# Kernel tuning notes

Hardware: AMD Instinct MI355X
Metric: run time of the kernel (lower is better)

Reference implementation:

```python
import jax, jax.numpy as jnp
import numpy as np

B, T, F = 8, 4096, 256

def setup_inputs() -> dict:
    key = jax.random.key(0)
    ks = jax.random.split(key, 10)
    s = 1.0 / np.sqrt(F)
    return {
        "x": jax.random.normal(ks[0], (B, T, F), dtype=jnp.float32),
        "Wq_w": jax.random.normal(ks[1], (F, F), dtype=jnp.float32) * s,
        "Wq_b": jax.random.normal(ks[2], (F,), dtype=jnp.float32) * 0.01,
        "Wk_w": jax.random.normal(ks[3], (F, F), dtype=jnp.float32) * s,
        "Wk_b": jax.random.normal(ks[4], (F,), dtype=jnp.float32) * 0.01,
        "Wv_w": jax.random.normal(ks[5], (F, F), dtype=jnp.float32) * s,
        "Wv_b": jax.random.normal(ks[6], (F,), dtype=jnp.float32) * 0.01,
        "w": jax.random.normal(ks[7], (T, T), dtype=jnp.float32) * 0.02,
        "out_w": jax.random.normal(ks[8], (F, F), dtype=jnp.float32) * s,
        "out_b": jax.random.normal(ks[9], (F,), dtype=jnp.float32) * 0.01,
    }

def reference(x, Wq_w, Wq_b, Wk_w, Wk_b, Wv_w, Wv_b, w, out_w, out_b):
    # Linear layers (torch convention: y = x @ W.T + b)
    Q = x @ Wq_w.T + Wq_b                      # [B, T, F]
    K = x @ Wk_w.T + Wk_b                      # [B, T, F]
    V = x @ Wv_w.T + Wv_b                      # [B, T, F]
    Q_sig = jax.nn.sigmoid(Q)
    # Stabilized exponentials (faithful: w over rows, K over FEATURE dim)
    exp_w = jnp.exp(w - jnp.max(w, axis=-1, keepdims=True))        # [T, T]
    exp_K = jnp.exp(K - jnp.max(K, axis=-1, keepdims=True))        # [B, T, F]
    num = jnp.einsum('ts,bsf->btf', exp_w, exp_K * V)              # [B, T, F]
    den = jnp.einsum('ts,bsf->btf', exp_w, exp_K)                  # [B, T, F]
    Yt = Q_sig * (num / den)
    return Yt @ out_w.T + out_b
```

## Files before the change

### kernel.cpp

```cpp
#include <hip/hip_runtime.h>
#include <hip/hip_bf16.h>

#define BB 8
#define TT 4096
#define FF 256
#define BT 32768

typedef unsigned short u16;
typedef __attribute__((ext_vector_type(8))) short short8;
typedef __attribute__((ext_vector_type(4))) float f32x4;
typedef __attribute__((ext_vector_type(4))) unsigned int u32x4;

static __device__ __forceinline__ float bf2f(u16 u) {
    union { unsigned int i; float f; } v; v.i = ((unsigned int)u) << 16; return v.f;
}
static __device__ __forceinline__ u16 f2bf(float f) {
    union { float f; unsigned int i; } v; v.f = f;
    unsigned int x = v.i;
    return (u16)((x + 0x7fffu + ((x >> 16) & 1u)) >> 16);
}

typedef const __attribute__((address_space(1))) void gvoid_t;
typedef __attribute__((address_space(3))) void svoid_t;

__global__ __launch_bounds__(256) void expw_kernel(const float* __restrict__ w,
                                                   u16* __restrict__ ew) {
    __shared__ float red[256];
    int row = blockIdx.x;
    int tid = threadIdx.x;
    const float* wr = w + (size_t)row * TT;

    f32x4 vals[4];
    float m = -1e30f;
#pragma unroll
    for (int v = 0; v < 4; ++v) {
        int idx = (v * 256 + tid) * 4;
        vals[v] = *(const f32x4*)(wr + idx);
#pragma unroll
        for (int j = 0; j < 4; ++j) m = fmaxf(m, vals[v][j]);
    }
    red[tid] = m;
    __syncthreads();
    for (int s = 128; s > 0; s >>= 1) {
        if (tid < s) red[tid] = fmaxf(red[tid], red[tid + s]);
        __syncthreads();
    }
    float rm = red[0];
#pragma unroll
    for (int v = 0; v < 4; ++v) {
        int idx = (v * 256 + tid) * 4;
        float e0 = expf(vals[v][0] - rm), e1 = expf(vals[v][1] - rm);
        float e2 = expf(vals[v][2] - rm), e3 = expf(vals[v][3] - rm);
        uint2 pk;
        pk.x = (unsigned int)f2bf(e0) | ((unsigned int)f2bf(e1) << 16);
        pk.y = (unsigned int)f2bf(e2) | ((unsigned int)f2bf(e3) << 16);
        *(uint2*)(ew + (size_t)row * TT + idx) = pk;
    }
}

__global__ __launch_bounds__(256) void cvt_bf16_kernel(const float* __restrict__ in,
                                                       u16* __restrict__ out, int n4) {
    int i = blockIdx.x * 256 + threadIdx.x;
    if (i < n4) {
        f32x4 v = ((const f32x4*)in)[i];
        uint2 pk;
        pk.x = (unsigned int)f2bf(v[0]) | ((unsigned int)f2bf(v[1]) << 16);
        pk.y = (unsigned int)f2bf(v[2]) | ((unsigned int)f2bf(v[3]) << 16);
        ((uint2*)out)[i] = pk;
    }
}

__global__ __launch_bounds__(256) void cvt_wkv_kernel(const float* __restrict__ wk,
                                                      const float* __restrict__ wv,
                                                      u16* __restrict__ wkv) {
    int i = blockIdx.x * 256 + threadIdx.x;
    if (i < FF * FF / 4) {
        int idx = i * 4;
        int f = idx >> 8, c = idx & 255;
        f32x4 a = *(const f32x4*)(wk + idx);
        f32x4 b = *(const f32x4*)(wv + idx);
        uint2 pa, pb;
        pa.x = (unsigned int)f2bf(a[0]) | ((unsigned int)f2bf(a[1]) << 16);
        pa.y = (unsigned int)f2bf(a[2]) | ((unsigned int)f2bf(a[3]) << 16);
        pb.x = (unsigned int)f2bf(b[0]) | ((unsigned int)f2bf(b[1]) << 16);
        pb.y = (unsigned int)f2bf(b[2]) | ((unsigned int)f2bf(b[3]) << 16);
        *(uint2*)(wkv + (size_t)(2 * f) * 256 + c) = pa;
        *(uint2*)(wkv + (size_t)(2 * f + 1) * 256 + c) = pb;
    }
}

template <int MODE>
__global__ __launch_bounds__(256) void gemm_nt(const u16* __restrict__ A,
                                               const u16* __restrict__ Bm,
                                               const float* __restrict__ bias,
                                               void* __restrict__ Call,
                                               int M, int N, int K) {
    __shared__ u16 As[128 * 32];
    __shared__ u16 Bs[128 * 32];

    int tid = threadIdx.x;
    int lane = tid & 63;
    int w = tid >> 6;
    int wr = w >> 1, wc = w & 1;
    int fr = lane & 15, kg = lane >> 4;

    f32x4 acc[4][4];
#pragma unroll
    for (int m = 0; m < 4; ++m)
#pragma unroll
        for (int n = 0; n < 4; ++n) acc[m][n] = (f32x4){0.f, 0.f, 0.f, 0.f};

    int bm = blockIdx.x, bn = blockIdx.y;
    int nk = K >> 5;

    int srow = tid >> 2;
    int schunk = (tid & 3) << 3;
    const u16* aBase = A + (size_t)(bm * 128 + srow) * K + schunk;
    const u16* bBase = Bm + (size_t)(bn * 128 + srow) * K + schunk;
    size_t half = (size_t)64 * K;

    for (int kt = 0; kt < nk; ++kt) {
        __syncthreads();
        int ko = kt << 5;
        __builtin_amdgcn_global_load_lds((gvoid_t*)(aBase + ko), (svoid_t*)&As[tid * 8], 16, 0, 0);
        __builtin_amdgcn_global_load_lds((gvoid_t*)(aBase + half + ko), (svoid_t*)&As[2048 + tid * 8], 16, 0, 0);
        __builtin_amdgcn_global_load_lds((gvoid_t*)(bBase + ko), (svoid_t*)&Bs[tid * 8], 16, 0, 0);
        __builtin_amdgcn_global_load_lds((gvoid_t*)(bBase + half + ko), (svoid_t*)&Bs[2048 + tid * 8], 16, 0, 0);
        __syncthreads();

        short8 af[4], bfr[4];
#pragma unroll
        for (int m = 0; m < 4; ++m)
            af[m] = *(const short8*)&As[(wr * 64 + m * 16 + fr) * 32 + kg * 8];
#pragma unroll
        for (int n = 0; n < 4; ++n)
            bfr[n] = *(const short8*)&Bs[(wc * 64 + n * 16 + fr) * 32 + kg * 8];
#pragma unroll
        for (int m = 0; m < 4; ++m)
#pragma unroll
            for (int n = 0; n < 4; ++n)
                acc[m][n] = __builtin_amdgcn_mfma_f32_16x16x32_bf16(af[m], bfr[n], acc[m][n], 0, 0, 0);
    }

    int row0 = bm * 128 + wr * 64;
    int col0 = bn * 128 + wc * 64;
#pragma unroll
    for (int n = 0; n < 4; ++n) {
        int col = col0 + n * 16 + fr;
        float bv = bias ? bias[col] : 0.0f;
#pragma unroll
        for (int m = 0; m < 4; ++m) {
            int rbase = row0 + m * 16 + kg * 4;
#pragma unroll
            for (int i = 0; i < 4; ++i) {
                float val = acc[m][n][i] + bv;
                size_t idx = (size_t)(rbase + i) * N + col;
                if (MODE == 0)
                    ((float*)Call)[idx] = val;
                else if (MODE == 1)
                    ((u16*)Call)[idx] = f2bf(1.0f / (1.0f + expf(-val)));
                else
                    ((u16*)Call)[idx] = f2bf(val);
            }
        }
    }
}

__global__ __launch_bounds__(512) void kv_mt_kernel(const u16* __restrict__ xbf,
                                                    const u16* __restrict__ wkv,
                                                    const float* __restrict__ bk,
                                                    const float* __restrict__ bv,
                                                    u16* __restrict__ mt) {
    __shared__ u16 As[128 * 32];
    __shared__ u16 Bs[512 * 32];
    __shared__ float rmax4[128][4];

    int tid = threadIdx.x;
    int lane = tid & 63, wid = tid >> 6;
    int fr = lane & 15, kg = lane >> 4;
    int wr = wid >> 2, wc = wid & 3;
    int row0g = blockIdx.x * 128;

    f32x4 acc[4][8];
#pragma unroll
    for (int m = 0; m < 4; ++m)
#pragma unroll
        for (int n = 0; n < 8; ++n) acc[m][n] = (f32x4){0.f, 0.f, 0.f, 0.f};

    const u16* aSrc = xbf + (size_t)(row0g + (tid >> 2)) * 256 + (tid & 3) * 8;
    const u16* bSrc = wkv + (size_t)(tid >> 2) * 256 + (tid & 3) * 8;

    for (int ks = 0; ks < 8; ++ks) {
        __syncthreads();
        __builtin_amdgcn_global_load_lds((gvoid_t*)(aSrc + ks * 32), (svoid_t*)&As[tid * 8], 16, 0, 0);
#pragma unroll
        for (int c = 0; c < 4; ++c)
            __builtin_amdgcn_global_load_lds((gvoid_t*)(bSrc + (size_t)c * 128 * 256 + ks * 32),
                                             (svoid_t*)&Bs[c * 4096 + tid * 8], 16, 0, 0);
        __syncthreads();

        short8 af[4], bfr[8];
#pragma unroll
        for (int m = 0; m < 4; ++m)
            af[m] = *(const short8*)&As[(wr * 64 + m * 16 + fr) * 32 + kg * 8];
#pragma unroll
        for (int n = 0; n < 8; ++n)
            bfr[n] = *(const short8*)&Bs[(wc * 128 + n * 16 + fr) * 32 + kg * 8];
#pragma unroll
        for (int m = 0; m < 4; ++m)
#pragma unroll
            for (int n = 0; n < 8; ++n)
                acc[m][n] = __builtin_amdgcn_mfma_f32_16x16x32_bf16(af[m], bfr[n], acc[m][n], 0, 0, 0);
    }

    int par = fr & 1;
#pragma unroll
    for (int n = 0; n < 8; ++n) {
        int col = wc * 128 + n * 16 + fr;
        int f = col >> 1;
        float bvv = par ? bv[f] : bk[f];
#pragma unroll
        for (int m = 0; m < 4; ++m)
#pragma unroll
            for (int i = 0; i < 4; ++i) acc[m][n][i] += bvv;
    }

    float rmax[4][4];
#pragma unroll
    for (int m = 0; m < 4; ++m)
#pragma unroll
        for (int i = 0; i < 4; ++i) {
            float mx = -1e30f;
#pragma unroll
            for (int n = 0; n < 8; ++n) mx = fmaxf(mx, par ? -1e30f : acc[m][n][i]);
            mx = fmaxf(mx, __shfl_xor(mx, 2));
            mx = fmaxf(mx, __shfl_xor(mx, 4));
            mx = fmaxf(mx, __shfl_xor(mx, 8));
            mx = fmaxf(mx, __shfl_xor(mx, 1));
            rmax[m][i] = mx;
        }
    if (fr == 0) {
#pragma unroll
        for (int m = 0; m < 4; ++m)
#pragma unroll
            for (int i = 0; i < 4; ++i)
                rmax4[wr * 64 + m * 16 + kg * 4 + i][wc] = rmax[m][i];
    }
    __syncthreads();
#pragma unroll
    for (int m = 0; m < 4; ++m)
#pragma unroll
        for (int i = 0; i < 4; ++i) {
            f32x4 r4 = *(const f32x4*)rmax4[wr * 64 + m * 16 + kg * 4 + i];
            rmax[m][i] = fmaxf(fmaxf(r4[0], r4[1]), fmaxf(r4[2], r4[3]));
        }

    int b = row0g >> 12;
    int tcb = (row0g & 4095) + wr * 64;
#pragma unroll
    for (int n = 0; n < 8; ++n) {
        int col = wc * 128 + n * 16 + fr;
        int f = col >> 1;
        size_t rowmt = (size_t)(b * 512 + 2 * f + (par ? 0 : 1));
#pragma unroll
        for (int m = 0; m < 4; ++m) {
            int tc = tcb + m * 16 + kg * 4;
            unsigned int w0, w1;
            u16 o[4];
#pragma unroll
            for (int i = 0; i < 4; ++i) {
                float v = acc[m][n][i];
                float ek = expf(v - rmax[m][i]);
                float ekx = __shfl_xor(ek, 1);
                float outv = par ? (ekx * v) : ek;
                o[i] = f2bf(outv);
            }
            w0 = (unsigned int)o[0] | ((unsigned int)o[1] << 16);
            w1 = (unsigned int)o[2] | ((unsigned int)o[3] << 16);
            uint2 pk = {w0, w1};
            *(uint2*)(mt + rowmt * TT + tc) = pk;
        }
    }
}

#define GLDS(src, eoff) \
    __builtin_amdgcn_global_load_lds((gvoid_t*)(src), (svoid_t*)&L[eoff], 16, 0, 0)

__global__ __launch_bounds__(512, 2) void gemm256_nt(const u16* __restrict__ A,
                                                     const u16* __restrict__ B,
                                                     const u16* __restrict__ qsig,
                                                     u16* __restrict__ yt) {
    __shared__ u16 L[65536];
    const int K = 4096, nt = 128;
    int tid = threadIdx.x;
    int lane = tid & 63, wid = tid >> 6;
    int fr = lane & 15, kg = lane >> 4;
    int wr = wid >> 2, wc = wid & 3;
    int bm = blockIdx.x, bn = blockIdx.y;

    int xpart = (((fr & 1) << 6) | (kg << 4)) ^ (((fr >> 1) & 7) << 4);
    int aoff = (wr * 64 + (fr >> 1)) * 128 + xpart;
    int boff = (wc * 32 + (fr >> 1)) * 128 + xpart;

    int l8 = lane >> 3;
    int v = (lane & 7) ^ l8;
    int srow = wid * 32 + l8 * 2 + (v >> 2);
    int scol = (v & 3) * 8;
    const u16* sA = A + (size_t)(bm * 256 + srow) * K + scol;
    const u16* sB = B + (size_t)(bn * 256 + srow) * K + scol;
    int dA = (wid * 2048) / 2 + lane * 8;
    int dB = dA + 32768;

    f32x4 acc[8][4];
#pragma unroll
    for (int m = 0; m < 8; ++m)
#pragma unroll
        for (int n = 0; n < 4; ++n) acc[m][n] = (f32x4){0.f, 0.f, 0.f, 0.f};

#pragma unroll
    for (int tt = 0; tt < 2; ++tt) {
        const u16* a = sA + tt * 32;
        const u16* b = sB + tt * 32;
        int qe = tt * 8192;
        GLDS(a, dA + qe);
        GLDS(a + 16 * K, dA + qe + 512);
        GLDS(b, dB + qe);
        GLDS(b + 16 * K, dB + qe + 512);
    }
    asm volatile("s_waitcnt vmcnt(4)" ::: "memory");
    __builtin_amdgcn_sched_barrier(0);
    __builtin_amdgcn_s_barrier();

    const char* LB = (const char*)L;
#pragma unroll 1
    for (int t = 0; t < nt; ++t) {
        int p = t & 3;
        int q = (t + 2) & 3;
        int ks = (t + 2 < nt) ? t + 2 : 0;
        int abase = p * 16384 + aoff;
        int bbase = 65536 + p * 16384 + boff;

        short8 af[8], bf4[4];
#pragma unroll
        for (int m = 0; m < 8; ++m) af[m] = *(const short8*)(LB + abase + m * 1024);
#pragma unroll
        for (int n = 0; n < 4; ++n) bf4[n] = *(const short8*)(LB + bbase + n * 1024);
        const u16* a = sA + ks * 32;
        GLDS(a, dA + q * 8192);
        GLDS(a + 16 * K, dA + q * 8192 + 512);
        asm volatile("s_waitcnt lgkmcnt(0)" ::: "memory");
        __builtin_amdgcn_sched_barrier(0);
        __builtin_amdgcn_s_setprio(1);
#pragma unroll
        for (int m = 0; m < 8; ++m)
#pragma unroll
            for (int n = 0; n < 2; ++n)
                acc[m][n] = __builtin_amdgcn_mfma_f32_16x16x32_bf16(af[m], bf4[n], acc[m][n], 0, 0, 0);
        __builtin_amdgcn_s_setprio(0);
        __builtin_amdgcn_s_barrier();

        const u16* b = sB + ks * 32;
        GLDS(b, dB + q * 8192);
        GLDS(b + 16 * K, dB + q * 8192 + 512);
        __builtin_amdgcn_s_setprio(1);
#pragma unroll
        for (int m = 0; m < 8; ++m)
#pragma unroll
            for (int n = 2; n < 4; ++n)
                acc[m][n] = __builtin_amdgcn_mfma_f32_16x16x32_bf16(af[m], bf4[n], acc[m][n], 0, 0, 0);
        __builtin_amdgcn_s_setprio(0);
        asm volatile("s_waitcnt vmcnt(4)" ::: "memory");
        __builtin_amdgcn_sched_barrier(0);
        __builtin_amdgcn_s_barrier();
    }

    int colgb = bn * 256 + wc * 64;
    int row0 = bm * 256 + wr * 128;
    bool isnum = ((fr & 1) == 0);
#pragma unroll
    for (int n = 0; n < 4; ++n) {
        int colg = colgb + n * 16 + fr;
        int b = colg >> 9;
        int f = (colg & 511) >> 1;
#pragma unroll
        for (int m = 0; m < 8; ++m) {
            int tr0 = row0 + m * 16 + kg * 4;
#pragma unroll
            for (int i = 0; i < 4; ++i) {
                float vv = acc[m][n][i];
                float other = __shfl_xor(vv, 1);
                if (isnum) {
                    size_t idx = ((size_t)(b * 4096 + tr0 + i) << 8) + f;
                    float qv = bf2f(qsig[idx]);
                    float r = qv * vv * __builtin_amdgcn_rcpf(other);
                    yt[idx] = f2bf(r);
                }
            }
        }
    }
}

extern "C" void kernel_launch(void* const* d_in, const int* in_sizes, int n_in,
                              void* d_out, int out_size, void* d_ws, size_t ws_size,
                              hipStream_t stream) {
    const float* x  = (const float*)d_in[0];
    const float* wq = (const float*)d_in[1];
    const float* bq = (const float*)d_in[2];
    const float* wk = (const float*)d_in[3];
    const float* bk = (const float*)d_in[4];
    const float* wv = (const float*)d_in[5];
    const float* bv = (const float*)d_in[6];
    const float* w  = (const float*)d_in[7];
    const float* wo = (const float*)d_in[8];
    const float* bo = (const float*)d_in[9];

    char* p = (char*)d_ws;
    u16* expw = (u16*)p; p += (size_t)TT * TT * 2;
    u16* xbf  = (u16*)p; p += (size_t)BT * FF * 2;
    u16* wqb  = (u16*)p; p += (size_t)FF * FF * 2;
    u16* wob  = (u16*)p; p += (size_t)FF * FF * 2;
    u16* wkv  = (u16*)p; p += (size_t)2 * FF * FF * 2;
    u16* qsig = (u16*)p; p += (size_t)BT * FF * 2;
    u16* mt   = (u16*)p; p += (size_t)BB * 512 * TT * 2;
    u16* yt = xbf;

    expw_kernel<<<TT, 256, 0, stream>>>(w, expw);

    cvt_bf16_kernel<<<(BT * FF / 4 + 255) / 256, 256, 0, stream>>>(x, xbf, BT * FF / 4);
    cvt_bf16_kernel<<<(FF * FF / 4 + 255) / 256, 256, 0, stream>>>(wq, wqb, FF * FF / 4);
    cvt_bf16_kernel<<<(FF * FF / 4 + 255) / 256, 256, 0, stream>>>(wo, wob, FF * FF / 4);
    cvt_wkv_kernel<<<(FF * FF / 4 + 255) / 256, 256, 0, stream>>>(wk, wv, wkv);

    dim3 gp(BT / 128, FF / 128, 1);
    gemm_nt<1><<<gp, 256, 0, stream>>>(xbf, wqb, bq, qsig, BT, FF, FF);

    kv_mt_kernel<<<BT / 128, 512, 0, stream>>>(xbf, wkv, bk, bv, mt);

    gemm256_nt<<<dim3(16, 16), 512, 0, stream>>>(expw, mt, qsig, yt);

    gemm_nt<0><<<gp, 256, 0, stream>>>(yt, wob, bo, (float*)d_out, BT, FF, FF);
}
```

Measured before the change: 207.1 us.

## Restructure big GEMM to K=64 double-buffered stages and fuse weight conversions

The main expw×mt GEMM now stages 64-wide K slices per iteration, double-buffered, instead of 32-wide slices in a four-slot ring. That halves the loop trip count and barriers, and uses a new XOR swizzle for LDS reads. Each iteration loads B fragments once and A fragments in two halves, and the epilogue is rebalanced so every lane writes two outputs instead of half the lanes idling. The three small weight-conversion launches are merged into one kernel to cut launch overhead. The risks are exposed load latency from waiting on vmcnt(0) each iteration and higher register pressure.

```diff
diff --git a/kernel.cpp b/kernel.cpp
--- a/kernel.cpp
+++ b/kernel.cpp
@@ -70,12 +70,29 @@
     }
 }
 
-__global__ __launch_bounds__(256) void cvt_wkv_kernel(const float* __restrict__ wk,
-                                                      const float* __restrict__ wv,
-                                                      u16* __restrict__ wkv) {
+__global__ __launch_bounds__(256) void cvt_weights_kernel(const float* __restrict__ wq,
+                                                          const float* __restrict__ wo,
+                                                          const float* __restrict__ wk,
+                                                          const float* __restrict__ wv,
+                                                          u16* __restrict__ wqb,
+                                                          u16* __restrict__ wob,
+                                                          u16* __restrict__ wkv) {
     int i = blockIdx.x * 256 + threadIdx.x;
-    if (i < FF * FF / 4) {
-        int idx = i * 4;
+    int which = i >> 14, j = i & 16383;
+    int idx = j * 4;
+    if (which == 0) {
+        f32x4 v = *(const f32x4*)(wq + idx);
+        uint2 pk;
+        pk.x = (unsigned int)f2bf(v[0]) | ((unsigned int)f2bf(v[1]) << 16);
+        pk.y = (unsigned int)f2bf(v[2]) | ((unsigned int)f2bf(v[3]) << 16);
+        *(uint2*)(wqb + idx) = pk;
+    } else if (which == 1) {
+        f32x4 v = *(const f32x4*)(wo + idx);
+        uint2 pk;
+        pk.x = (unsigned int)f2bf(v[0]) | ((unsigned int)f2bf(v[1]) << 16);
+        pk.y = (unsigned int)f2bf(v[2]) | ((unsigned int)f2bf(v[3]) << 16);
+        *(uint2*)(wob + idx) = pk;
+    } else {
         int f = idx >> 8, c = idx & 255;
         f32x4 a = *(const f32x4*)(wk + idx);
         f32x4 b = *(const f32x4*)(wv + idx);
@@ -265,7 +282,6 @@
 #pragma unroll
         for (int m = 0; m < 4; ++m) {
             int tc = tcb + m * 16 + kg * 4;
-            unsigned int w0, w1;
             u16 o[4];
 #pragma unroll
             for (int i = 0; i < 4; ++i) {
@@ -275,9 +291,9 @@
                 float outv = par ? (ekx * v) : ek;
                 o[i] = f2bf(outv);
             }
-            w0 = (unsigned int)o[0] | ((unsigned int)o[1] << 16);
-            w1 = (unsigned int)o[2] | ((unsigned int)o[3] << 16);
-            uint2 pk = {w0, w1};
+            uint2 pk;
+            pk.x = (unsigned int)o[0] | ((unsigned int)o[1] << 16);
+            pk.y = (unsigned int)o[2] | ((unsigned int)o[3] << 16);
             *(uint2*)(mt + rowmt * TT + tc) = pk;
         }
     }
@@ -285,31 +301,39 @@
 
 #define GLDS(src, eoff) \
     __builtin_amdgcn_global_load_lds((gvoid_t*)(src), (svoid_t*)&L[eoff], 16, 0, 0)
+
+#define STAGE8(P_, KS_) do {                                                   \
+    _Pragma("unroll")                                                          \
+    for (int i_ = 0; i_ < 4; ++i_) {                                           \
+        GLDS(sA + (size_t)i_ * 64 * 4096 + (KS_) * 64,                         \
+             (P_) * 16384 + i_ * 4096 + dst);                                  \
+        GLDS(sB + (size_t)i_ * 64 * 4096 + (KS_) * 64,                         \
+             32768 + (P_) * 16384 + i_ * 4096 + dst);                          \
+    }                                                                          \
+} while (0)
 
 __global__ __launch_bounds__(512, 2) void gemm256_nt(const u16* __restrict__ A,
                                                      const u16* __restrict__ B,
                                                      const u16* __restrict__ qsig,
                                                      u16* __restrict__ yt) {
     __shared__ u16 L[65536];
-    const int K = 4096, nt = 128;
+    const int K = 4096;
     int tid = threadIdx.x;
     int lane = tid & 63, wid = tid >> 6;
     int fr = lane & 15, kg = lane >> 4;
     int wr = wid >> 2, wc = wid & 3;
     int bm = blockIdx.x, bn = blockIdx.y;
-
-    int xpart = (((fr & 1) << 6) | (kg << 4)) ^ (((fr >> 1) & 7) << 4);
-    int aoff = (wr * 64 + (fr >> 1)) * 128 + xpart;
-    int boff = (wc * 32 + (fr >> 1)) * 128 + xpart;
-
-    int l8 = lane >> 3;
-    int v = (lane & 7) ^ l8;
-    int srow = wid * 32 + l8 * 2 + (v >> 2);
-    int scol = (v & 3) * 8;
-    const u16* sA = A + (size_t)(bm * 256 + srow) * K + scol;
-    const u16* sB = B + (size_t)(bn * 256 + srow) * K + scol;
-    int dA = (wid * 2048) / 2 + lane * 8;
-    int dB = dA + 32768;
+    const char* LB = (const char*)L;
+
+    int x0 = (kg * 16) ^ ((fr & 7) << 4);
+    int x1 = (64 + kg * 16) ^ ((fr & 7) << 4);
+    int arow = (wr * 128 + fr) * 128;
+    int brow = (wc * 64 + fr) * 128;
+
+    int scol = ((tid & 7) * 8) ^ (((tid >> 3) & 7) << 3);
+    const u16* sA = A + (size_t)(bm * 256 + (tid >> 3)) * K + scol;
+    const u16* sB = B + (size_t)(bn * 256 + (tid >> 3)) * K + scol;
+    int dst = tid * 8;
 
     f32x4 acc[8][4];
 #pragma unroll
@@ -317,66 +341,68 @@
 #pragma unroll
         for (int n = 0; n < 4; ++n) acc[m][n] = (f32x4){0.f, 0.f, 0.f, 0.f};
 
-#pragma unroll
-    for (int tt = 0; tt < 2; ++tt) {
-        const u16* a = sA + tt * 32;
-        const u16* b = sB + tt * 32;
-        int qe = tt * 8192;
-        GLDS(a, dA + qe);
-        GLDS(a + 16 * K, dA + qe + 512);
-        GLDS(b, dB + qe);
-        GLDS(b + 16 * K, dB + qe + 512);
-    }
-    asm volatile("s_waitcnt vmcnt(4)" ::: "memory");
+    STAGE8(0, 0);
+    asm volatile("s_waitcnt vmcnt(0)" ::: "memory");
     __builtin_amdgcn_sched_barrier(0);
     __builtin_amdgcn_s_barrier();
 
-    const char* LB = (const char*)L;
 #pragma unroll 1
-    for (int t = 0; t < nt; ++t) {
-        int p = t & 3;
-        int q = (t + 2) & 3;
-        int ks = (t + 2 < nt) ? t + 2 : 0;
-        int abase = p * 16384 + aoff;
-        int bbase = 65536 + p * 16384 + boff;
-
-        short8 af[8], bf4[4];
-#pragma unroll
-        for (int m = 0; m < 8; ++m) af[m] = *(const short8*)(LB + abase + m * 1024);
-#pragma unroll
-        for (int n = 0; n < 4; ++n) bf4[n] = *(const short8*)(LB + bbase + n * 1024);
-        const u16* a = sA + ks * 32;
-        GLDS(a, dA + q * 8192);
-        GLDS(a + 16 * K, dA + q * 8192 + 512);
+    for (int t = 0; t < 64; ++t) {
+        int p = t & 1;
+        const char* abase = LB + p * 32768;
+        const char* bbase = LB + 65536 + p * 32768;
+
+        short8 bfr[4][2], af[4][2];
+#pragma unroll
+        for (int nf = 0; nf < 4; ++nf) {
+            const char* rb = bbase + brow + nf * 2048;
+            bfr[nf][0] = *(const short8*)(rb + x0);
+            bfr[nf][1] = *(const short8*)(rb + x1);
+        }
+#pragma unroll
+        for (int mf = 0; mf < 4; ++mf) {
+            const char* rb = abase + arow + mf * 2048;
+            af[mf][0] = *(const short8*)(rb + x0);
+            af[mf][1] = *(const short8*)(rb + x1);
+        }
+        int ks = (t + 1 < 64) ? t + 1 : 0;
+        STAGE8(p ^ 1, ks);
         asm volatile("s_waitcnt lgkmcnt(0)" ::: "memory");
         __builtin_amdgcn_sched_barrier(0);
         __builtin_amdgcn_s_setprio(1);
 #pragma unroll
-        for (int m = 0; m < 8; ++m)
-#pragma unroll
-            for (int n = 0; n < 2; ++n)
-                acc[m][n] = __builtin_amdgcn_mfma_f32_16x16x32_bf16(af[m], bf4[n], acc[m][n], 0, 0, 0);
+        for (int mf = 0; mf < 4; ++mf)
+#pragma unroll
+            for (int nf = 0; nf < 4; ++nf) {
+                acc[mf][nf] = __builtin_amdgcn_mfma_f32_16x16x32_bf16(af[mf][0], bfr[nf][0], acc[mf][nf], 0, 0, 0);
+                acc[mf][nf] = __builtin_amdgcn_mfma_f32_16x16x32_bf16(af[mf][1], bfr[nf][1], acc[mf][nf], 0, 0, 0);
+            }
         __builtin_amdgcn_s_setprio(0);
-        __builtin_amdgcn_s_barrier();
-
-        const u16* b = sB + ks * 32;
-        GLDS(b, dB + q * 8192);
-        GLDS(b + 16 * K, dB + q * 8192 + 512);
+#pragma unroll
+        for (int mf = 0; mf < 4; ++mf) {
+            const char* rb = abase + arow + (mf + 4) * 2048;
+            af[mf][0] = *(const short8*)(rb + x0);
+            af[mf][1] = *(const short8*)(rb + x1);
+        }
+        asm volatile("s_waitcnt lgkmcnt(0)" ::: "memory");
+        __builtin_amdgcn_sched_barrier(0);
         __builtin_amdgcn_s_setprio(1);
 #pragma unroll
-        for (int m = 0; m < 8; ++m)
-#pragma unroll
-            for (int n = 2; n < 4; ++n)
-                acc[m][n] = __builtin_amdgcn_mfma_f32_16x16x32_bf16(af[m], bf4[n], acc[m][n], 0, 0, 0);
+        for (int mf = 0; mf < 4; ++mf)
+#pragma unroll
+            for (int nf = 0; nf < 4; ++nf) {
+                acc[mf + 4][nf] = __builtin_amdgcn_mfma_f32_16x16x32_bf16(af[mf][0], bfr[nf][0], acc[mf + 4][nf], 0, 0, 0);
+                acc[mf + 4][nf] = __builtin_amdgcn_mfma_f32_16x16x32_bf16(af[mf][1], bfr[nf][1], acc[mf + 4][nf], 0, 0, 0);
+            }
         __builtin_amdgcn_s_setprio(0);
-        asm volatile("s_waitcnt vmcnt(4)" ::: "memory");
+        asm volatile("s_waitcnt vmcnt(0)" ::: "memory");
         __builtin_amdgcn_sched_barrier(0);
         __builtin_amdgcn_s_barrier();
     }
 
     int colgb = bn * 256 + wc * 64;
     int row0 = bm * 256 + wr * 128;
-    bool isnum = ((fr & 1) == 0);
+    int par = fr & 1;
 #pragma unroll
     for (int n = 0; n < 4; ++n) {
         int colg = colgb + n * 16 + fr;
@@ -385,17 +411,19 @@
 #pragma unroll
         for (int m = 0; m < 8; ++m) {
             int tr0 = row0 + m * 16 + kg * 4;
-#pragma unroll
-            for (int i = 0; i < 4; ++i) {
-                float vv = acc[m][n][i];
-                float other = __shfl_xor(vv, 1);
-                if (isnum) {
-                    size_t idx = ((size_t)(b * 4096 + tr0 + i) << 8) + f;
-                    float qv = bf2f(qsig[idx]);
-                    float r = qv * vv * __builtin_amdgcn_rcpf(other);
-                    yt[idx] = f2bf(r);
-                }
-            }
+            float v0 = acc[m][n][0], v1 = acc[m][n][1];
+            float v2 = acc[m][n][2], v3 = acc[m][n][3];
+            float o0 = __shfl_xor(v0, 1), o1 = __shfl_xor(v1, 1);
+            float o2 = __shfl_xor(v2, 1), o3 = __shfl_xor(v3, 1);
+            float nA = par ? o2 : v0, dA = par ? v2 : o0;
+            float nB = par ? o3 : v1, dB = par ? v3 : o1;
+            int iA = par ? 2 : 0;
+            size_t idxA = ((size_t)(b * 4096 + tr0 + iA) << 8) + f;
+            size_t idxB = idxA + 256;
+            float qA = bf2f(qsig[idxA]);
+            float qB = bf2f(qsig[idxB]);
+            yt[idxA] = f2bf(qA * nA * __builtin_amdgcn_rcpf(dA));
+            yt[idxB] = f2bf(qB * nB * __builtin_amdgcn_rcpf(dB));
         }
     }
 }
@@ -427,9 +455,7 @@
     expw_kernel<<<TT, 256, 0, stream>>>(w, expw);
 
     cvt_bf16_kernel<<<(BT * FF / 4 + 255) / 256, 256, 0, stream>>>(x, xbf, BT * FF / 4);
-    cvt_bf16_kernel<<<(FF * FF / 4 + 255) / 256, 256, 0, stream>>>(wq, wqb, FF * FF / 4);
-    cvt_bf16_kernel<<<(FF * FF / 4 + 255) / 256, 256, 0, stream>>>(wo, wob, FF * FF / 4);
-    cvt_wkv_kernel<<<(FF * FF / 4 + 255) / 256, 256, 0, stream>>>(wk, wv, wkv);
+    cvt_weights_kernel<<<192, 256, 0, stream>>>(wq, wo, wk, wv, wqb, wob, wkv);
 
     dim3 gp(BT / 128, FF / 128, 1);
     gemm_nt<1><<<gp, 256, 0, stream>>>(xbf, wqb, bq, qsig, BT, FF, FF);
```

New measurement: 187.6 us. 9.4% less time.
